# Optimization experiments

Measured on AMD Instinct MI355X. Metric: run time of the kernel, lower is better.

## Reference

```python
import jax, jax.numpy as jnp
import numpy as np

B, Q, KV = 8, 16, 2048
NQ, NK, NV, H = 512, 512, 512, 512

def setup_inputs() -> dict:
    key = jax.random.key(0)
    k = jax.random.split(key, 7)
    s = 0.02
    return {
        "query": jax.random.normal(k[0], (B, Q, NQ), jnp.float32),
        "keys": jax.random.normal(k[1], (B, KV, NK), jnp.float32),
        "values": jax.random.normal(k[2], (B, KV, NV), jnp.float32),
        "W_weight": jax.random.normal(k[3], (H, NQ + NK), jnp.float32) * s,
        "W_bias": jax.random.normal(k[4], (H,), jnp.float32) * s,
        "v_weight": jax.random.normal(k[5], (1, H), jnp.float32) * s,
        "v_bias": jax.random.normal(k[6], (1,), jnp.float32) * s,
    }

def reference(query, keys, values, W_weight, W_bias, v_weight, v_bias):
    # Split W over the concat axis: cat([query, keys]) @ W^T == query@Wq^T + keys@Wk^T
    Wq = W_weight[:, :NQ]   # [H, Nq]
    Wk = W_weight[:, NQ:]   # [H, Nk]
    q_part = jnp.einsum('bqn,hn->bqh', query, Wq)   # [B,Q,H]
    k_part = jnp.einsum('bkn,hn->bkh', keys, Wk)    # [B,KV,H]
    # broadcast-add -> [B,KV,Q,H], tanh, project to scalar energy
    energy = jnp.tanh(k_part[:, :, None, :] + q_part[:, None, :, :] + W_bias)
    e = jnp.einsum('bkqh,h->bkq', energy, v_weight[0]) + v_bias[0]  # [B,KV,Q]
    scores = jax.nn.softmax(e, axis=1)              # softmax over KV
    # output = (values^T @ scores)^T -> [B,Q,Nv]
    output = jnp.einsum('bkn,bkq->bqn', values, scores)
    return output
```

## Files before the change

### kernel.cpp

```cpp
#include <hip/hip_runtime.h>
#include <cstddef>

using bf16x8  = __attribute__((ext_vector_type(8))) short;
using short4v = __attribute__((ext_vector_type(4))) short;
using f32x4   = __attribute__((ext_vector_type(4))) float;
using ushort8 = __attribute__((ext_vector_type(8))) unsigned short;

#define GLL16(gp, lp) __builtin_amdgcn_global_load_lds( \
    (const __attribute__((address_space(1))) unsigned int*)(const void*)(gp), \
    (__attribute__((address_space(3))) unsigned int*)(void*)(lp), 16, 0, 0)

__device__ __forceinline__ float exp2_f(float x){ float r; asm("v_exp_f32 %0, %1" : "=v"(r) : "v"(x)); return r; }
__device__ __forceinline__ float rcp_f (float x){ float r; asm("v_rcp_f32 %0, %1" : "=v"(r) : "v"(x)); return r; }
__device__ __forceinline__ unsigned pk2(float lo, float hi){
  unsigned r; asm("v_cvt_pk_bf16_f32 %0, %1, %2" : "=v"(r) : "v"(lo), "v"(hi)); return r;
}
__device__ __forceinline__ unsigned short f2bf(float f){
  unsigned int u = __float_as_uint(f);
  u = u + 0x7FFFu + ((u >> 16) & 1u);
  return (unsigned short)(u >> 16);
}
__device__ __forceinline__ float bf2f(unsigned short s){
  return __uint_as_float(((unsigned int)s) << 16);
}

#define QUAD(E, k0v,k1v,k2v,k3v, w0v,w1v,w2v,w3v, a) { \
  const float d0 = fmaf((k0v), (E).x, 1.f); \
  const float d1 = fmaf((k1v), (E).y, 1.f); \
  const float d2 = fmaf((k2v), (E).z, 1.f); \
  const float d3 = fmaf((k3v), (E).w, 1.f); \
  const float p01 = d0 * d1, p23 = d2 * d3; \
  const float n01 = fmaf((w1v), d0, (w0v) * d1); \
  const float n23 = fmaf((w3v), d2, (w2v) * d3); \
  (a) = fmaf(fmaf(n01, p23, n23 * p01), rcp_f(p01 * p23), (a)); }

#define QG_BLOCKS 16
#define WK_BLOCKS 128
#define SCALE_2LOG2E 2.885390081777927f

#define OFF_WK_BF     0u
#define OFF_EQB       524288u
#define OFF_EPART     786432u
#define OFF_SC        4980736u

__global__ __launch_bounds__(256) void k_convert(
    const float* __restrict__ W, const float* __restrict__ query,
    unsigned short* __restrict__ wk_bf, float* __restrict__ eqb)
{
  __shared__ short qg[128*32 + 32*32];
  if (blockIdx.x < QG_BLOCKS) {
    const int n0 = blockIdx.x * 32;
    const int tid = threadIdx.x;
    const int l = tid & 63, w = tid >> 6;
    short* A  = qg;
    short* Bs = qg + 4096;
    const int sub = tid >> 3;
    const int c4  = (tid & 7) * 4;
    const int wm = w & 1, wn = w >> 1;
    const int fr = l & 15, fg = l >> 4;

    f32x4 acc[4];
    #pragma unroll
    for (int i = 0; i < 4; ++i) acc[i] = (f32x4){0.f,0.f,0.f,0.f};

    float4 a4[4], b4, a4n[4], b4n;
    #pragma unroll
    for (int m = 0; m < 4; ++m)
      a4[m] = *(const float4*)(query + (size_t)(m * 32 + sub) * 512 + c4);
    b4 = *(const float4*)(W + (size_t)(n0 + sub) * 1024 + c4);

    for (int kt = 0; kt < 16; ++kt) {
      if (kt < 15) {
        const int k0 = (kt + 1) * 32;
        #pragma unroll
        for (int m = 0; m < 4; ++m)
          a4n[m] = *(const float4*)(query + (size_t)(m * 32 + sub) * 512 + k0 + c4);
        b4n = *(const float4*)(W + (size_t)(n0 + sub) * 1024 + k0 + c4);
      }
      __syncthreads();
      #pragma unroll
      for (int m = 0; m < 4; ++m) {
        const int row = m * 32 + sub;
        const int o = row * 32 + (((c4 >> 3) ^ ((row >> 1) & 3)) << 3) + (c4 & 7);
        *(uint2*)&A[o] = make_uint2(pk2(a4[m].x, a4[m].y), pk2(a4[m].z, a4[m].w));
      }
      {
        const int o = sub * 32 + (((c4 >> 3) ^ ((sub >> 1) & 3)) << 3) + (c4 & 7);
        *(uint2*)&Bs[o] = make_uint2(pk2(b4.x, b4.y), pk2(b4.z, b4.w));
      }
      __syncthreads();
      bf16x8 af[4], bfv;
      #pragma unroll
      for (int i = 0; i < 4; ++i) {
        const int ar = wm*64 + i*16 + fr;
        af[i] = *(const bf16x8*)&A[ar*32 + ((fg ^ ((ar>>1)&3)) << 3)];
      }
      const int br = wn*16 + fr;
      bfv = *(const bf16x8*)&Bs[br*32 + ((fg ^ ((br>>1)&3)) << 3)];
      #pragma unroll
      for (int i = 0; i < 4; ++i)
        acc[i] = __builtin_amdgcn_mfma_f32_16x16x32_bf16(af[i], bfv, acc[i], 0, 0, 0);
      if (kt < 15) {
        #pragma unroll
        for (int m = 0; m < 4; ++m) a4[m] = a4n[m];
        b4 = b4n;
      }
    }
    const int gh = n0 + wn*16 + fr;
    #pragma unroll
    for (int i = 0; i < 4; ++i)
      #pragma unroll
      for (int r = 0; r < 4; ++r) {
        const int gm = wm*64 + i*16 + fg*4 + r;
        eqb[gm * 512 + gh] = exp2_f(acc[i][r] * SCALE_2LOG2E);
      }
    return;
  }
  int e = (blockIdx.x - QG_BLOCKS) * 2048 + threadIdx.x * 8;
  const float* src = W + (size_t)(e >> 9) * 1024 + 512 + (e & 511);
  float4 a = *(const float4*)src;
  float4 b = *(const float4*)(src + 4);
  ushort8 o;
  o[0]=f2bf(a.x); o[1]=f2bf(a.y); o[2]=f2bf(a.z); o[3]=f2bf(a.w);
  o[4]=f2bf(b.x); o[5]=f2bf(b.y); o[6]=f2bf(b.z); o[7]=f2bf(b.w);
  *(ushort8*)&wk_bf[e] = o;
}

struct FusedSM {
  union {
    struct { short A[2][8192]; short B[2][8192]; } g;
    unsigned short ekbf[128 * 128];
  } u;
  float eqs[16 * 128];
};

__global__ __launch_bounds__(256, 2) void k_fused(
    const float* __restrict__ keys, const unsigned short* __restrict__ wk_bf,
    const float* __restrict__ w_bias, const float* __restrict__ eqb,
    const float* __restrict__ vw, float* __restrict__ e_part)
{
  __shared__ FusedSM sm;
  const int tid = threadIdx.x;
  const int l = tid & 63, w = tid >> 6;
  const int by = blockIdx.x;
  const int hc = blockIdx.y;
  const int h0 = hc * 128;
  const int b  = by >> 4;

  {
    const int q = tid >> 4, c0 = (tid & 15) * 8;
    const float* src = eqb + (size_t)(b * 16 + q) * 512 + h0 + c0;
    *(float4*)&sm.eqs[q * 128 + c0]     = *(const float4*)src;
    *(float4*)&sm.eqs[q * 128 + c0 + 4] = *(const float4*)(src + 4);
  }
  asm volatile("s_waitcnt vmcnt(0)" ::: "memory");

  const float* Akeys = keys + (size_t)by * 128 * 512;
  const unsigned short* Bptr = wk_bf + (size_t)h0 * 512;

  const int srow = w * 32 + (l >> 3);
  const int scol = ((l & 7) ^ (l >> 3)) * 8;
  const int wm = w >> 1, wn = w & 1;
  const int fr = l & 15, fg = l >> 4;
  const int axk = fr & 7;

  f32x4 acc[4][4];
  #pragma unroll
  for (int i = 0; i < 4; ++i)
    #pragma unroll
    for (int j = 0; j < 4; ++j) acc[i][j] = (f32x4){0.f,0.f,0.f,0.f};

  float4 areg[8];
  auto aload = [&](int kt) {
    const float* src = Akeys + kt * 64;
    #pragma unroll
    for (int m = 0; m < 8; ++m) {
      const int u = m * 256 + tid;
      areg[m] = *(const float4*)(src + (size_t)(u >> 4) * 512 + (u & 15) * 4);
    }
  };
  auto awrite = [&](int buf) {
    #pragma unroll
    for (int m = 0; m < 8; ++m) {
      const int u = m * 256 + tid;
      const int row = u >> 4, c4 = u & 15;
      const int o = row * 64 + (((c4 >> 1) ^ (row & 7)) << 3) + (c4 & 1) * 4;
      *(uint2*)&sm.u.g.A[buf][o] =
          make_uint2(pk2(areg[m].x, areg[m].y), pk2(areg[m].z, areg[m].w));
    }
  };
  auto bstage = [&](int buf, int kt) {
    const int k0 = kt * 64;
    #pragma unroll
    for (int r = 0; r < 4; ++r)
      GLL16(Bptr + (srow + r * 8) * 512 + k0 + scol, &sm.u.g.B[buf][w * 2048 + r * 512]);
  };
  auto compute = [&](int buf) {
    #pragma unroll
    for (int ks = 0; ks < 2; ++ks) {
      bf16x8 af[4], bfv[4];
      #pragma unroll
      for (int i = 0; i < 4; ++i) {
        af[i]  = *(const bf16x8*)&sm.u.g.A[buf][(wm*64 + i*16 + fr) * 64 + ((ks*4 + fg) ^ axk) * 8];
        bfv[i] = *(const bf16x8*)&sm.u.g.B[buf][(wn*64 + i*16 + fr) * 64 + ((ks*4 + fg) ^ axk) * 8];
      }
      #pragma unroll
      for (int i = 0; i < 4; ++i)
        #pragma unroll
        for (int j = 0; j < 4; ++j)
          acc[i][j] = __builtin_amdgcn_mfma_f32_16x16x32_bf16(af[i], bfv[j], acc[i][j], 0, 0, 0);
    }
  };

  aload(0);
  asm volatile("s_waitcnt vmcnt(0)" ::: "memory");
  awrite(0);
  bstage(0, 0);

  #pragma unroll 1
  for (int kt = 0; kt < 8; ++kt) {
    if (kt < 7) {
      aload(kt + 1);
      asm volatile("s_waitcnt vmcnt(8)" ::: "memory");
    } else {
      asm volatile("s_waitcnt vmcnt(0)" ::: "memory");
    }
    asm volatile("s_waitcnt lgkmcnt(0)" ::: "memory");
    __builtin_amdgcn_sched_barrier(0);
    __builtin_amdgcn_s_barrier();
    __builtin_amdgcn_sched_barrier(0);
    if (kt < 7) bstage((kt + 1) & 1, kt + 1);
    compute(kt & 1);
    if (kt < 7) {
      asm volatile("s_waitcnt vmcnt(4)" ::: "memory");
      __builtin_amdgcn_sched_barrier(0);
      awrite((kt + 1) & 1);
    }
  }
  asm volatile("s_waitcnt lgkmcnt(0)" ::: "memory");
  __builtin_amdgcn_sched_barrier(0);
  __builtin_amdgcn_s_barrier();
  __builtin_amdgcn_sched_barrier(0);

  #pragma unroll
  for (int j = 0; j < 4; ++j) {
    const int col = wn*64 + j*16 + fr;
    const float bias = w_bias[h0 + col];
    const int chunk = col >> 3, coff = col & 7;
    #pragma unroll
    for (int i = 0; i < 4; ++i)
      #pragma unroll
      for (int r = 0; r < 4; ++r) {
        const int row = wm*64 + i*16 + fg*4 + r;
        const float ev = exp2_f((acc[i][j][r] + bias) * SCALE_2LOG2E);
        sm.u.ekbf[row * 128 + ((chunk ^ (fg*4 + r)) << 3) + coff] = f2bf(ev);
      }
  }
  const int g = l & 3, kl = l >> 2;
  float vv[32];
  #pragma unroll
  for (int s = 0; s < 4; ++s) {
    const float4 a0 = *(const float4*)(vw + h0 + s*32 + g*4);
    const float4 a1 = *(const float4*)(vw + h0 + s*32 + 16 + g*4);
    vv[s*8+0]=-2.f*a0.x; vv[s*8+1]=-2.f*a0.y; vv[s*8+2]=-2.f*a0.z; vv[s*8+3]=-2.f*a0.w;
    vv[s*8+4]=-2.f*a1.x; vv[s*8+5]=-2.f*a1.y; vv[s*8+6]=-2.f*a1.z; vv[s*8+7]=-2.f*a1.w;
  }
  __syncthreads();

  {
    const int lr0 = w * 32 + kl;
    const int lr1 = lr0 + 16;
    float ek0[32], ek1[32];
    #pragma unroll
    for (int s = 0; s < 4; ++s)
      #pragma unroll
      for (int hf = 0; hf < 2; ++hf) {
        const int ck = (4*s + 2*hf + (g >> 1)) ^ kl;
        const short4v v40 = *(const short4v*)&sm.u.ekbf[lr0 * 128 + (ck << 3) + (g & 1) * 4];
        const short4v v41 = *(const short4v*)&sm.u.ekbf[lr1 * 128 + (ck << 3) + (g & 1) * 4];
        #pragma unroll
        for (int u = 0; u < 4; ++u) {
          ek0[s*8 + hf*4 + u] = bf2f((unsigned short)v40[u]);
          ek1[s*8 + hf*4 + u] = bf2f((unsigned short)v41[u]);
        }
      }
    const size_t ep0 = (size_t)hc * 262144 + ((size_t)(by * 128 + lr0)) * 16;
    const size_t ep1 = (size_t)hc * 262144 + ((size_t)(by * 128 + lr1)) * 16;
    #pragma unroll 4
    for (int q = 0; q < 16; ++q) {
      float a00 = 0.f, a01 = 0.f, a10 = 0.f, a11 = 0.f;
      #pragma unroll
      for (int s = 0; s < 4; ++s) {
        const float* er = &sm.eqs[q * 128 + s * 32 + g * 4];
        const float4 E0 = *(const float4*)er;
        const float4 E1 = *(const float4*)(er + 16);
        QUAD(E0, ek0[s*8+0],ek0[s*8+1],ek0[s*8+2],ek0[s*8+3],
                 vv[s*8+0],vv[s*8+1],vv[s*8+2],vv[s*8+3], a00);
        QUAD(E1, ek0[s*8+4],ek0[s*8+5],ek0[s*8+6],ek0[s*8+7],
                 vv[s*8+4],vv[s*8+5],vv[s*8+6],vv[s*8+7], a01);
        QUAD(E0, ek1[s*8+0],ek1[s*8+1],ek1[s*8+2],ek1[s*8+3],
                 vv[s*8+0],vv[s*8+1],vv[s*8+2],vv[s*8+3], a10);
        QUAD(E1, ek1[s*8+4],ek1[s*8+5],ek1[s*8+6],ek1[s*8+7],
                 vv[s*8+4],vv[s*8+5],vv[s*8+6],vv[s*8+7], a11);
      }
      float r0 = a00 + a01;
      r0 += __shfl_xor(r0, 1, 64);
      r0 += __shfl_xor(r0, 2, 64);
      float r1 = a10 + a11;
      r1 += __shfl_xor(r1, 1, 64);
      r1 += __shfl_xor(r1, 2, 64);
      if (g == 0) { e_part[ep0 + q] = r0; e_part[ep1 + q] = r1; }
    }
  }
}

__global__ __launch_bounds__(256) void k_softmax(
    const float* __restrict__ e_part, float* __restrict__ sc)
{
  const int b = blockIdx.x >> 4, q = blockIdx.x & 15;
  const int base = b * 32768 + q;
  const int tid = threadIdx.x;
  __shared__ float redm[4], reds[4];

  float vals[8];
  float mx = -1e30f;
  #pragma unroll
  for (int i = 0; i < 8; ++i) {
    const int x = base + (tid + i * 256) * 16;
    vals[i] = (e_part[x] + e_part[x + 262144]) + (e_part[x + 524288] + e_part[x + 786432]);
    mx = fmaxf(mx, vals[i]);
  }
  #pragma unroll
  for (int msk = 1; msk < 64; msk <<= 1) mx = fmaxf(mx, __shfl_xor(mx, msk, 64));
  if ((tid & 63) == 0) redm[tid >> 6] = mx;
  __syncthreads();
  mx = fmaxf(fmaxf(redm[0], redm[1]), fmaxf(redm[2], redm[3]));

  float ex[8], sum = 0.f;
  #pragma unroll
  for (int i = 0; i < 8; ++i) { ex[i] = __expf(vals[i] - mx); sum += ex[i]; }
  #pragma unroll
  for (int msk = 1; msk < 64; msk <<= 1) sum += __shfl_xor(sum, msk, 64);
  if ((tid & 63) == 0) reds[tid >> 6] = sum;
  __syncthreads();
  sum = reds[0] + reds[1] + reds[2] + reds[3];
  const float r = 1.f / sum;
  #pragma unroll
  for (int i = 0; i < 8; ++i) sc[base + (tid + i * 256) * 16] = ex[i] * r;
}

__global__ __launch_bounds__(512) void k_pv(
    const float* __restrict__ values, const float* __restrict__ sc,
    float* __restrict__ out)
{
  __shared__ float lds[128 * 20];
  const int tid = threadIdx.x;
  const int nc = blockIdx.x & 31, b = blockIdx.x >> 5;
  const int n = tid & 15, kg = tid >> 4;
  const int l = tid & 63, w = tid >> 6;
  const int n0 = nc * 16;

  float acc[16];
  #pragma unroll
  for (int q = 0; q < 16; ++q) acc[q] = 0.f;

  for (int kc = 0; kc < 16; ++kc) {
    __syncthreads();
    {
      const float* ssrc = sc + (size_t)(b * 2048 + kc * 128) * 16;
      const int row = tid >> 2, c4 = (tid & 3) * 4;
      *(float4*)&lds[row * 20 + c4] = *(const float4*)&ssrc[row * 16 + c4];
    }
    __syncthreads();
    const float* vb = values + ((size_t)(b * 2048 + kc * 128 + kg * 4)) * 512 + n0 + n;
    #pragma unroll
    for (int k2 = 0; k2 < 4; ++k2) {
      const float v = vb[(size_t)k2 * 512];
      const float* sr = &lds[(kg * 4 + k2) * 20];
      #pragma unroll
      for (int qq = 0; qq < 4; ++qq) {
        const float4 s4 = *(const float4*)&sr[qq * 4];
        acc[qq*4+0] = fmaf(v, s4.x, acc[qq*4+0]);
        acc[qq*4+1] = fmaf(v, s4.y, acc[qq*4+1]);
        acc[qq*4+2] = fmaf(v, s4.z, acc[qq*4+2]);
        acc[qq*4+3] = fmaf(v, s4.w, acc[qq*4+3]);
      }
    }
  }
  #pragma unroll
  for (int q = 0; q < 16; ++q) {
    acc[q] += __shfl_xor(acc[q], 16, 64);
    acc[q] += __shfl_xor(acc[q], 32, 64);
  }
  __syncthreads();
  if (l < 16) {
    #pragma unroll
    for (int q = 0; q < 16; ++q) lds[w * 256 + q * 16 + l] = acc[q];
  }
  __syncthreads();
  if (tid < 256) {
    const int q = tid >> 4, nn = tid & 15;
    float s = 0.f;
    #pragma unroll
    for (int w2 = 0; w2 < 8; ++w2) s += lds[w2 * 256 + q * 16 + nn];
    out[((size_t)(b * 16 + q)) * 512 + n0 + nn] = s;
  }
}

extern "C" void kernel_launch(void* const* d_in, const int* in_sizes, int n_in,
                              void* d_out, int out_size, void* d_ws, size_t ws_size,
                              hipStream_t stream)
{
  const float* query  = (const float*)d_in[0];
  const float* keys   = (const float*)d_in[1];
  const float* values = (const float*)d_in[2];
  const float* W      = (const float*)d_in[3];
  const float* w_bias = (const float*)d_in[4];
  const float* vw     = (const float*)d_in[5];

  char* ws = (char*)d_ws;
  unsigned short* wk_bf = (unsigned short*)(ws + OFF_WK_BF);
  float* eqb    = (float*)(ws + OFF_EQB);
  float* e_part = (float*)(ws + OFF_EPART);
  float* sc     = (float*)(ws + OFF_SC);

  hipLaunchKernelGGL(k_convert, dim3(QG_BLOCKS + WK_BLOCKS), dim3(256), 0, stream,
                     W, query, wk_bf, eqb);
  hipLaunchKernelGGL(k_fused, dim3(128, 4), dim3(256), 0, stream,
                     keys, wk_bf, w_bias, eqb, vw, e_part);
  hipLaunchKernelGGL(k_softmax, dim3(128), dim3(256), 0, stream, e_part, sc);
  hipLaunchKernelGGL(k_pv, dim3(256), dim3(512), 0, stream, values, sc, (float*)d_out);
}
```

Baseline: 82.88 us.

## Halve H chunk per fused block to raise occupancy and restructure keys pipeline

```diff
diff --git a/kernel.cpp b/kernel.cpp
--- a/kernel.cpp
+++ b/kernel.cpp
@@ -41,7 +41,7 @@
 #define OFF_WK_BF     0u
 #define OFF_EQB       524288u
 #define OFF_EPART     786432u
-#define OFF_SC        4980736u
+#define OFF_SC        9175040u
 
 __global__ __launch_bounds__(256) void k_convert(
     const float* __restrict__ W, const float* __restrict__ query,
@@ -128,13 +128,14 @@
 
 struct FusedSM {
   union {
-    struct { short A[2][8192]; short B[2][8192]; } g;
-    unsigned short ekbf[128 * 128];
+    short A[8192];
+    unsigned short ekbf[128 * 64];
   } u;
-  float eqs[16 * 128];
+  short B[2][4096];
+  float eqs[16 * 64];
 };
 
-__global__ __launch_bounds__(256, 2) void k_fused(
+__global__ __launch_bounds__(256, 4) void k_fused(
     const float* __restrict__ keys, const unsigned short* __restrict__ wk_bf,
     const float* __restrict__ w_bias, const float* __restrict__ eqb,
     const float* __restrict__ vw, float* __restrict__ e_part)
@@ -144,31 +145,21 @@
   const int l = tid & 63, w = tid >> 6;
   const int by = blockIdx.x;
   const int hc = blockIdx.y;
-  const int h0 = hc * 128;
+  const int h0 = hc * 64;
   const int b  = by >> 4;
-
-  {
-    const int q = tid >> 4, c0 = (tid & 15) * 8;
-    const float* src = eqb + (size_t)(b * 16 + q) * 512 + h0 + c0;
-    *(float4*)&sm.eqs[q * 128 + c0]     = *(const float4*)src;
-    *(float4*)&sm.eqs[q * 128 + c0 + 4] = *(const float4*)(src + 4);
-  }
-  asm volatile("s_waitcnt vmcnt(0)" ::: "memory");
 
   const float* Akeys = keys + (size_t)by * 128 * 512;
   const unsigned short* Bptr = wk_bf + (size_t)h0 * 512;
 
-  const int srow = w * 32 + (l >> 3);
-  const int scol = ((l & 7) ^ (l >> 3)) * 8;
   const int wm = w >> 1, wn = w & 1;
   const int fr = l & 15, fg = l >> 4;
   const int axk = fr & 7;
 
-  f32x4 acc[4][4];
+  f32x4 acc[4][2];
   #pragma unroll
   for (int i = 0; i < 4; ++i)
     #pragma unroll
-    for (int j = 0; j < 4; ++j) acc[i][j] = (f32x4){0.f,0.f,0.f,0.f};
+    for (int j = 0; j < 2; ++j) acc[i][j] = (f32x4){0.f,0.f,0.f,0.f};
 
   float4 areg[8];
   auto aload = [&](int kt) {
@@ -179,72 +170,85 @@
       areg[m] = *(const float4*)(src + (size_t)(u >> 4) * 512 + (u & 15) * 4);
     }
   };
-  auto awrite = [&](int buf) {
+  auto awrite = [&]() {
     #pragma unroll
     for (int m = 0; m < 8; ++m) {
       const int u = m * 256 + tid;
       const int row = u >> 4, c4 = u & 15;
       const int o = row * 64 + (((c4 >> 1) ^ (row & 7)) << 3) + (c4 & 1) * 4;
-      *(uint2*)&sm.u.g.A[buf][o] =
+      *(uint2*)&sm.u.A[o] =
           make_uint2(pk2(areg[m].x, areg[m].y), pk2(areg[m].z, areg[m].w));
     }
   };
   auto bstage = [&](int buf, int kt) {
     const int k0 = kt * 64;
     #pragma unroll
-    for (int r = 0; r < 4; ++r)
-      GLL16(Bptr + (srow + r * 8) * 512 + k0 + scol, &sm.u.g.B[buf][w * 2048 + r * 512]);
+    for (int m = 0; m < 2; ++m) {
+      const int u = m * 256 + tid;
+      const int row = u >> 3, chunk = u & 7;
+      GLL16(Bptr + (size_t)row * 512 + k0 + ((chunk ^ (row & 7)) << 3),
+            &sm.B[buf][(m * 256 + (w << 6)) * 8 + 0] + (l << 3));
+    }
   };
   auto compute = [&](int buf) {
     #pragma unroll
     for (int ks = 0; ks < 2; ++ks) {
-      bf16x8 af[4], bfv[4];
+      bf16x8 af[4], bfv[2];
       #pragma unroll
       for (int i = 0; i < 4; ++i) {
-        af[i]  = *(const bf16x8*)&sm.u.g.A[buf][(wm*64 + i*16 + fr) * 64 + ((ks*4 + fg) ^ axk) * 8];
-        bfv[i] = *(const bf16x8*)&sm.u.g.B[buf][(wn*64 + i*16 + fr) * 64 + ((ks*4 + fg) ^ axk) * 8];
+        const int ar = wm*64 + i*16 + fr;
+        af[i] = *(const bf16x8*)&sm.u.A[ar*64 + ((ks*4 + fg) ^ axk) * 8];
+      }
+      #pragma unroll
+      for (int j = 0; j < 2; ++j) {
+        const int br = wn*32 + j*16 + fr;
+        bfv[j] = *(const bf16x8*)&sm.B[buf][br*64 + ((ks*4 + fg) ^ axk) * 8];
       }
       #pragma unroll
       for (int i = 0; i < 4; ++i)
         #pragma unroll
-        for (int j = 0; j < 4; ++j)
+        for (int j = 0; j < 2; ++j)
           acc[i][j] = __builtin_amdgcn_mfma_f32_16x16x32_bf16(af[i], bfv[j], acc[i][j], 0, 0, 0);
     }
   };
 
   aload(0);
-  asm volatile("s_waitcnt vmcnt(0)" ::: "memory");
-  awrite(0);
+  {
+    const int q = tid >> 4, c0 = (tid & 15) * 4;
+    const float4 e4 = *(const float4*)(eqb + (size_t)(b * 16 + q) * 512 + h0 + c0);
+    asm volatile("s_waitcnt vmcnt(0)" ::: "memory");
+    *(float4*)&sm.eqs[q * 64 + c0] = e4;
+  }
+  awrite();
   bstage(0, 0);
+  aload(1);
+  asm volatile("s_waitcnt lgkmcnt(0)" ::: "memory");
 
   #pragma unroll 1
   for (int kt = 0; kt < 8; ++kt) {
-    if (kt < 7) {
-      aload(kt + 1);
-      asm volatile("s_waitcnt vmcnt(8)" ::: "memory");
-    } else {
-      asm volatile("s_waitcnt vmcnt(0)" ::: "memory");
-    }
+    if (kt < 7) asm volatile("s_waitcnt vmcnt(8)" ::: "memory");
+    else        asm volatile("s_waitcnt vmcnt(0)" ::: "memory");
+    __builtin_amdgcn_sched_barrier(0);
+    __builtin_amdgcn_s_barrier();
+    __builtin_amdgcn_sched_barrier(0);
+    compute(kt & 1);
     asm volatile("s_waitcnt lgkmcnt(0)" ::: "memory");
     __builtin_amdgcn_sched_barrier(0);
     __builtin_amdgcn_s_barrier();
     __builtin_amdgcn_sched_barrier(0);
-    if (kt < 7) bstage((kt + 1) & 1, kt + 1);
-    compute(kt & 1);
     if (kt < 7) {
-      asm volatile("s_waitcnt vmcnt(4)" ::: "memory");
+      asm volatile("s_waitcnt vmcnt(0)" ::: "memory");
+      awrite();
+      bstage((kt + 1) & 1, kt + 1);
+      if (kt < 6) aload(kt + 2);
+      asm volatile("s_waitcnt lgkmcnt(0)" ::: "memory");
       __builtin_amdgcn_sched_barrier(0);
-      awrite((kt + 1) & 1);
-    }
-  }
-  asm volatile("s_waitcnt lgkmcnt(0)" ::: "memory");
-  __builtin_amdgcn_sched_barrier(0);
-  __builtin_amdgcn_s_barrier();
-  __builtin_amdgcn_sched_barrier(0);
-
-  #pragma unroll
-  for (int j = 0; j < 4; ++j) {
-    const int col = wn*64 + j*16 + fr;
+    }
+  }
+
+  #pragma unroll
+  for (int j = 0; j < 2; ++j) {
+    const int col = wn*32 + j*16 + fr;
     const float bias = w_bias[h0 + col];
     const int chunk = col >> 3, coff = col & 7;
     #pragma unroll
@@ -253,31 +257,32 @@
       for (int r = 0; r < 4; ++r) {
         const int row = wm*64 + i*16 + fg*4 + r;
         const float ev = exp2_f((acc[i][j][r] + bias) * SCALE_2LOG2E);
-        sm.u.ekbf[row * 128 + ((chunk ^ (fg*4 + r)) << 3) + coff] = f2bf(ev);
+        sm.u.ekbf[row * 64 + ((chunk ^ ((fg*4 + r) & 7)) << 3) + coff] = f2bf(ev);
       }
   }
   const int g = l & 3, kl = l >> 2;
-  float vv[32];
-  #pragma unroll
-  for (int s = 0; s < 4; ++s) {
-    const float4 a0 = *(const float4*)(vw + h0 + s*32 + g*4);
-    const float4 a1 = *(const float4*)(vw + h0 + s*32 + 16 + g*4);
-    vv[s*8+0]=-2.f*a0.x; vv[s*8+1]=-2.f*a0.y; vv[s*8+2]=-2.f*a0.z; vv[s*8+3]=-2.f*a0.w;
-    vv[s*8+4]=-2.f*a1.x; vv[s*8+5]=-2.f*a1.y; vv[s*8+6]=-2.f*a1.z; vv[s*8+7]=-2.f*a1.w;
-  }
+  float vv[16];
+  #pragma unroll
+  for (int s = 0; s < 2; ++s)
+    #pragma unroll
+    for (int hf = 0; hf < 2; ++hf) {
+      const float4 a4 = *(const float4*)(vw + h0 + s*32 + hf*16 + g*4);
+      const int o = s*8 + hf*4;
+      vv[o+0]=-2.f*a4.x; vv[o+1]=-2.f*a4.y; vv[o+2]=-2.f*a4.z; vv[o+3]=-2.f*a4.w;
+    }
   __syncthreads();
 
   {
     const int lr0 = w * 32 + kl;
     const int lr1 = lr0 + 16;
-    float ek0[32], ek1[32];
-    #pragma unroll
-    for (int s = 0; s < 4; ++s)
+    float ek0[16], ek1[16];
+    #pragma unroll
+    for (int s = 0; s < 2; ++s)
       #pragma unroll
       for (int hf = 0; hf < 2; ++hf) {
-        const int ck = (4*s + 2*hf + (g >> 1)) ^ kl;
-        const short4v v40 = *(const short4v*)&sm.u.ekbf[lr0 * 128 + (ck << 3) + (g & 1) * 4];
-        const short4v v41 = *(const short4v*)&sm.u.ekbf[lr1 * 128 + (ck << 3) + (g & 1) * 4];
+        const int ck = (s*4 + hf*2 + (g >> 1)) ^ (kl & 7);
+        const short4v v40 = *(const short4v*)&sm.u.ekbf[lr0 * 64 + (ck << 3) + (g & 1) * 4];
+        const short4v v41 = *(const short4v*)&sm.u.ekbf[lr1 * 64 + (ck << 3) + (g & 1) * 4];
         #pragma unroll
         for (int u = 0; u < 4; ++u) {
           ek0[s*8 + hf*4 + u] = bf2f((unsigned short)v40[u]);
@@ -290,8 +295,8 @@
     for (int q = 0; q < 16; ++q) {
       float a00 = 0.f, a01 = 0.f, a10 = 0.f, a11 = 0.f;
       #pragma unroll
-      for (int s = 0; s < 4; ++s) {
-        const float* er = &sm.eqs[q * 128 + s * 32 + g * 4];
+      for (int s = 0; s < 2; ++s) {
+        const float* er = &sm.eqs[q * 64 + s * 32 + g * 4];
         const float4 E0 = *(const float4*)er;
         const float4 E1 = *(const float4*)(er + 16);
         QUAD(E0, ek0[s*8+0],ek0[s*8+1],ek0[s*8+2],ek0[s*8+3],
@@ -327,7 +332,10 @@
   #pragma unroll
   for (int i = 0; i < 8; ++i) {
     const int x = base + (tid + i * 256) * 16;
-    vals[i] = (e_part[x] + e_part[x + 262144]) + (e_part[x + 524288] + e_part[x + 786432]);
+    float s = 0.f;
+    #pragma unroll
+    for (int p = 0; p < 8; ++p) s += e_part[x + p * 262144];
+    vals[i] = s;
     mx = fmaxf(mx, vals[i]);
   }
   #pragma unroll
@@ -426,7 +434,7 @@
 
   hipLaunchKernelGGL(k_convert, dim3(QG_BLOCKS + WK_BLOCKS), dim3(256), 0, stream,
                      W, query, wk_bf, eqb);
-  hipLaunchKernelGGL(k_fused, dim3(128, 4), dim3(256), 0, stream,
+  hipLaunchKernelGGL(k_fused, dim3(128, 8), dim3(256), 0, stream,
                      keys, wk_bf, w_bias, eqb, vw, e_part);
   hipLaunchKernelGGL(k_softmax, dim3(128), dim3(256), 0, stream, e_part, sc);
   hipLaunchKernelGGL(k_pv, dim3(256), dim3(512), 0, stream, values, sc, (float*)d_out);
```

Result: slower. 96.92 us (+16.9%).
